# Kernel tuning notes

Measured on AMD Instinct MI355X. Metric: run time of the kernel, lower is better.

Reference implementation:

```python
import jax, jax.numpy as jnp
import numpy as np

N = 50000      # nodes
E = 800000     # edges (avg degree 16)
F_IN = 256     # input features
H = 128        # hidden
C = 40         # classes


def setup_inputs() -> dict:
    key = jax.random.key(0)
    ks = jax.random.split(key, 10)
    features = jax.random.normal(ks[0], (N, F_IN), dtype=jnp.float32)
    src = jax.random.randint(ks[1], (E,), 0, N, dtype=jnp.int32)
    dst = jax.random.randint(ks[2], (E,), 0, N, dtype=jnp.int32)
    edge_weights = jax.random.uniform(ks[3], (E,), dtype=jnp.float32)
    def glorot(k, i, o):
        return jax.random.normal(k, (i, o), dtype=jnp.float32) * np.float32(1.0 / np.sqrt(i))
    W1 = glorot(ks[4], F_IN, H); b1 = jnp.zeros((H,), jnp.float32)
    W2 = glorot(ks[5], H, H);    b2 = jnp.zeros((H,), jnp.float32)
    W3 = glorot(ks[6], H, C);    b3 = jnp.zeros((C,), jnp.float32)
    return dict(features=features, src=src, dst=dst, edge_weights=edge_weights,
                W1=W1, b1=b1, W2=W2, b2=b2, W3=W3, b3=b3)


def _gcn_layer(h, src, dst, ew, out_norm, in_norm, W, b, act):
    # norm='both': pre-scale by out_degree^-0.5, post-scale by in_degree^-0.5
    h = h * out_norm[:, None]
    in_gt_out = W.shape[0] > W.shape[1]
    if in_gt_out:
        h = h @ W                      # matmul first (in_feats > out_feats)
    # message = u_mul_e, reduce = sum  (SpMM-style gather-scale-scatter)
    agg = jax.ops.segment_sum(h[src] * ew[:, None], dst, num_segments=N)
    if not in_gt_out:
        agg = agg @ W                  # aggregate first (in_feats <= out_feats)
    agg = agg * in_norm[:, None] + b
    return act(agg) if act is not None else agg


def reference(features, src, dst, edge_weights, W1, b1, W2, b2, W3, b3):
    ones = jnp.ones((E,), jnp.float32)
    out_deg = jnp.clip(jax.ops.segment_sum(ones, src, num_segments=N), 1.0)
    in_deg = jnp.clip(jax.ops.segment_sum(ones, dst, num_segments=N), 1.0)
    out_norm = out_deg ** -0.5
    in_norm = in_deg ** -0.5
    relu = jax.nn.relu
    # dropout is identity in eval mode
    h = _gcn_layer(features, src, dst, edge_weights, out_norm, in_norm, W1, b1, relu)
    h = _gcn_layer(h, src, dst, edge_weights, out_norm, in_norm, W2, b2, relu)
    h = _gcn_layer(h, src, dst, edge_weights, out_norm, in_norm, W3, b3, None)
    return h
```

## Files before the change

kernel.cpp:

```cpp
#include <hip/hip_runtime.h>
#include <hip/hip_bf16.h>
#include <cstdint>


#define F_IN 256
#define HDIM 128
#define CDIM 40
#define RBITS 13
#define RSIZE 8192
#define NSUB 64

typedef short bf16x8 __attribute__((ext_vector_type(8)));
typedef float f32x4  __attribute__((ext_vector_type(4)));

__device__ __forceinline__ ushort f2bf(float x) {
    uint b = __float_as_uint(x);
    return (ushort)((b + 0x7fffu + ((b >> 16) & 1u)) >> 16);
}
__device__ __forceinline__ float bf2f(ushort h) {
    return __uint_as_float(((uint)h) << 16);
}

__global__ __launch_bounds__(256)
void histo_range(const int* __restrict__ src, const int* __restrict__ dst,
                 int* __restrict__ pc, int E) {
    __shared__ int h[RSIZE];
    const int s = blockIdx.x;
    const int r = blockIdx.y;
    const int base = r << RBITS;
    const int t = threadIdx.x;
    int4* h4 = reinterpret_cast<int4*>(h);
    for (int j = t; j < RSIZE / 4; j += 256) h4[j] = make_int4(0, 0, 0, 0);
    __syncthreads();

    const int ech = (E + NSUB - 1) / NSUB;
    const int e0 = s * ech;
    const int e1 = min(E, e0 + ech);
    const int n4 = (e1 - e0) >> 2;
    for (int g = t; g < n4; g += 256) {
        int4 d4 = *reinterpret_cast<const int4*>(dst + e0 + g * 4);
        int4 s4 = *reinterpret_cast<const int4*>(src + e0 + g * 4);
        #pragma unroll
        for (int j = 0; j < 4; ++j) {
            int d = (&d4.x)[j] - base;
            int v = (&s4.x)[j] - base;
            if ((unsigned)d < RSIZE) atomicAdd(&h[d], 1);
            if ((unsigned)v < RSIZE) atomicAdd(&h[v], 0x10000);
        }
    }
    for (int e = e0 + n4 * 4 + t; e < e1; e += 256) {
        int d = dst[e] - base, v = src[e] - base;
        if ((unsigned)d < RSIZE) atomicAdd(&h[d], 1);
        if ((unsigned)v < RSIZE) atomicAdd(&h[v], 0x10000);
    }
    __syncthreads();
    int* p = pc + ((size_t)r * NSUB + s) * RSIZE;
    for (int j = t; j < RSIZE; j += 256) p[j] = h[j];
}

__global__ __launch_bounds__(256)
void scan_blocks(const int* __restrict__ pc, int* __restrict__ out,
                 int* __restrict__ bsums, int n) {
    const int t = threadIdx.x;
    const int idx = blockIdx.x * 1024 + t * 4;
    int4 v = make_int4(0, 0, 0, 0);
    if (idx + 3 < n) {
        const int r = idx >> RBITS, off = idx & (RSIZE - 1);
        const int* p = pc + (size_t)r * NSUB * RSIZE + off;
        #pragma unroll 8
        for (int c = 0; c < NSUB; ++c) {
            int4 u = *reinterpret_cast<const int4*>(p + (size_t)c * RSIZE);
            v.x += u.x & 0xffff; v.y += u.y & 0xffff;
            v.z += u.z & 0xffff; v.w += u.w & 0xffff;
        }
    } else {
        for (int j = 0; j < 4; ++j) {
            if (idx + j < n) {
                const int r = (idx + j) >> RBITS, off = (idx + j) & (RSIZE - 1);
                int s = 0;
                for (int c = 0; c < NSUB; ++c)
                    s += pc[(size_t)r * NSUB * RSIZE + (size_t)c * RSIZE + off] & 0xffff;
                (&v.x)[j] = s;
            }
        }
    }
    const int s = v.x + v.y + v.z + v.w;
    const int lane = t & 63;
    int incl = s;
    #pragma unroll
    for (int off = 1; off < 64; off <<= 1) {
        int u = __shfl_up(incl, off);
        if (lane >= off) incl += u;
    }
    __shared__ int wsum[4];
    if (lane == 63) wsum[t >> 6] = incl;
    __syncthreads();
    const int w = t >> 6;
    int woff = 0;
    if (w > 0) woff += wsum[0];
    if (w > 1) woff += wsum[1];
    if (w > 2) woff += wsum[2];
    const int excl = woff + incl - s;
    if (idx + 3 < n) {
        *reinterpret_cast<int4*>(out + idx) =
            make_int4(excl, excl + v.x, excl + v.x + v.y, excl + v.x + v.y + v.z);
    } else {
        if (idx     < n) out[idx]     = excl;
        if (idx + 1 < n) out[idx + 1] = excl + v.x;
        if (idx + 2 < n) out[idx + 2] = excl + v.x + v.y;
        if (idx + 3 < n) out[idx + 3] = excl + v.x + v.y + v.z;
    }
    if (t == 255) bsums[blockIdx.x] = woff + incl;
}

__global__ __launch_bounds__(64)
void scan_sums(int* __restrict__ bsums, int nb) {
    const int lane = threadIdx.x & 63;
    int carry = 0;
    for (int base = 0; base < nb; base += 64) {
        int v = (base + lane < nb) ? bsums[base + lane] : 0;
        int incl = v;
        #pragma unroll
        for (int off = 1; off < 64; off <<= 1) {
            int u = __shfl_up(incl, off);
            if (lane >= off) incl += u;
        }
        if (base + lane < nb) bsums[base + lane] = carry + incl - v;
        carry += __shfl(incl, 63);
    }
}

__global__ __launch_bounds__(256)
void node_prep_kernel(const int* __restrict__ pc,
                      int* __restrict__ row_ptr, const int* __restrict__ bsums,
                      float* __restrict__ out_norm, float* __restrict__ in_norm,
                      int* __restrict__ cb, int n, int E) {
    int i = blockIdx.x * 256 + threadIdx.x;
    if (i < n) {
        const int r = i >> RBITS, off = i & (RSIZE - 1);
        const int* p = pc + (size_t)r * NSUB * RSIZE + off;
        int rp = row_ptr[i] + bsums[i >> 10];
        row_ptr[i] = rp;
        int cur = rp;
        int od = 0;
        #pragma unroll 8
        for (int c = 0; c < NSUB; ++c) {
            unsigned pv = (unsigned)p[(size_t)c * RSIZE];
            cb[(size_t)c * n + i] = cur;
            cur += (int)(pv & 0xffffu);
            od  += (int)(pv >> 16);
        }
        int id = cur - rp;
        out_norm[i] = rsqrtf((float)max(od, 1));
        in_norm[i]  = rsqrtf((float)max(id, 1));
    }
    if (i == 0) row_ptr[n] = E;
}

__global__ __launch_bounds__(256)
void scatter_range(const int* __restrict__ src, const int* __restrict__ dst,
                   const float* __restrict__ ew, const float* __restrict__ out_norm,
                   const int* __restrict__ cb, int2* __restrict__ edges,
                   int E, int N) {
    __shared__ int cur[RSIZE];
    const int s = blockIdx.x;
    const int r = blockIdx.y;
    const int base = r << RBITS;
    const int t = threadIdx.x;
    for (int j = t; j < RSIZE; j += 256)
        if (base + j < N) cur[j] = cb[(size_t)s * N + base + j];
    __syncthreads();

    const int ech = (E + NSUB - 1) / NSUB;
    const int e0 = s * ech;
    const int e1 = min(E, e0 + ech);
    const int n4 = (e1 - e0) >> 2;
    for (int g = t; g < n4; g += 256) {
        int4 d4 = *reinterpret_cast<const int4*>(dst + e0 + g * 4);
        int4 s4 = *reinterpret_cast<const int4*>(src + e0 + g * 4);
        float4 w4 = *reinterpret_cast<const float4*>(ew + e0 + g * 4);
        #pragma unroll
        for (int j = 0; j < 4; ++j) {
            int d = (&d4.x)[j] - base;
            if ((unsigned)d < RSIZE) {
                int sv = (&s4.x)[j];
                int pos = atomicAdd(&cur[d], 1);
                float w = (&w4.x)[j] * out_norm[sv];
                edges[pos] = make_int2(sv, __float_as_int(w));
            }
        }
    }
    for (int e = e0 + n4 * 4 + t; e < e1; e += 256) {
        int d = dst[e] - base;
        if ((unsigned)d < RSIZE) {
            int sv = src[e];
            int pos = atomicAdd(&cur[d], 1);
            float w = ew[e] * out_norm[sv];
            edges[pos] = make_int2(sv, __float_as_int(w));
        }
    }
}

__global__ __launch_bounds__(256)
void conv_w(const float* __restrict__ W, ushort* __restrict__ Wt_hi,
            ushort* __restrict__ Wt_lo, int K) {
    int i = blockIdx.x * 256 + threadIdx.x;
    if (i < K * 128) {
        int k = i >> 7, n = i & 127;
        float x = W[i];
        ushort hi = f2bf(x);
        ushort lo = f2bf(x - bf2f(hi));
        Wt_hi[(size_t)n * K + k] = hi;
        Wt_lo[(size_t)n * K + k] = lo;
    }
}

template <int MODE>
__global__ __launch_bounds__(256)
void gemm128_mfma(const float* __restrict__ A, const ushort* __restrict__ Wt_hi,
                  const ushort* __restrict__ Wt_lo, float* __restrict__ C,
                  int M, int K,
                  const float* __restrict__ rownorm, const float* __restrict__ bias) {
    constexpr int BK = 32;
    constexpr int AP = 40;
    __shared__ __align__(16) ushort As_hi[64 * AP];
    __shared__ __align__(16) ushort As_lo[64 * AP];
    __shared__ __align__(16) ushort Bs_hi[128 * AP];
    __shared__ __align__(16) ushort Bs_lo[128 * AP];

    const int t = threadIdx.x;
    const int w = t >> 6;
    const int l = t & 63;
    const int row0 = blockIdx.x * 64;

    const int ar = t >> 2;
    const int ak = (t & 3) * 8;
    const int bn = t >> 1;
    const int bko = (t & 1) * 16;

    const int fr = l & 15;
    const int fk = (l >> 4) * 8;

    f32x4 acc[8];
    #pragma unroll
    for (int i = 0; i < 8; ++i) acc[i] = (f32x4){0.f, 0.f, 0.f, 0.f};

    const bool arow_ok = (row0 + ar < M);
    const float* ap = A + (size_t)(row0 + ar) * K;

    for (int k0 = 0; k0 < K; k0 += BK) {
        float av[8];
        if (arow_ok) {
            float4 f0 = *reinterpret_cast<const float4*>(ap + k0 + ak);
            float4 f1 = *reinterpret_cast<const float4*>(ap + k0 + ak + 4);
            av[0] = f0.x; av[1] = f0.y; av[2] = f0.z; av[3] = f0.w;
            av[4] = f1.x; av[5] = f1.y; av[6] = f1.z; av[7] = f1.w;
        } else {
            #pragma unroll
            for (int j = 0; j < 8; ++j) av[j] = 0.f;
        }
        bf16x8 ah, al;
        #pragma unroll
        for (int j = 0; j < 8; ++j) {
            ushort hi = f2bf(av[j]);
            ah[j] = (short)hi;
            al[j] = (short)f2bf(av[j] - bf2f(hi));
        }
        const ushort* wh = Wt_hi + (size_t)bn * K + k0 + bko;
        const ushort* wl = Wt_lo + (size_t)bn * K + k0 + bko;
        bf16x8 bh0 = *reinterpret_cast<const bf16x8*>(wh);
        bf16x8 bh1 = *reinterpret_cast<const bf16x8*>(wh + 8);
        bf16x8 bl0 = *reinterpret_cast<const bf16x8*>(wl);
        bf16x8 bl1 = *reinterpret_cast<const bf16x8*>(wl + 8);

        __syncthreads();
        *reinterpret_cast<bf16x8*>(As_hi + ar * AP + ak) = ah;
        *reinterpret_cast<bf16x8*>(As_lo + ar * AP + ak) = al;
        *reinterpret_cast<bf16x8*>(Bs_hi + bn * AP + bko)     = bh0;
        *reinterpret_cast<bf16x8*>(Bs_hi + bn * AP + bko + 8) = bh1;
        *reinterpret_cast<bf16x8*>(Bs_lo + bn * AP + bko)     = bl0;
        *reinterpret_cast<bf16x8*>(Bs_lo + bn * AP + bko + 8) = bl1;
        __syncthreads();

        bf16x8 a_hi = *reinterpret_cast<const bf16x8*>(As_hi + (w * 16 + fr) * AP + fk);
        bf16x8 a_lo = *reinterpret_cast<const bf16x8*>(As_lo + (w * 16 + fr) * AP + fk);
        #pragma unroll
        for (int nt = 0; nt < 8; ++nt) {
            bf16x8 b_hi = *reinterpret_cast<const bf16x8*>(Bs_hi + (nt * 16 + fr) * AP + fk);
            bf16x8 b_lo = *reinterpret_cast<const bf16x8*>(Bs_lo + (nt * 16 + fr) * AP + fk);
            acc[nt] = __builtin_amdgcn_mfma_f32_16x16x32_bf16(a_hi, b_hi, acc[nt], 0, 0, 0);
            acc[nt] = __builtin_amdgcn_mfma_f32_16x16x32_bf16(a_hi, b_lo, acc[nt], 0, 0, 0);
            acc[nt] = __builtin_amdgcn_mfma_f32_16x16x32_bf16(a_lo, b_hi, acc[nt], 0, 0, 0);
        }
    }

    float bb[8];
    if (MODE == 1) {
        #pragma unroll
        for (int nt = 0; nt < 8; ++nt) bb[nt] = bias[nt * 16 + fr];
    }
    #pragma unroll
    for (int r = 0; r < 4; ++r) {
        int row = row0 + w * 16 + (l >> 4) * 4 + r;
        if (row >= M) continue;
        float rn = (MODE == 1) ? rownorm[row] : 0.f;
        float* cp = C + (size_t)row * 128;
        #pragma unroll
        for (int nt = 0; nt < 8; ++nt) {
            float v = acc[nt][r];
            if (MODE == 1) v = fmaxf(fmaf(v, rn, bb[nt]), 0.f);
            cp[nt * 16 + fr] = v;
        }
    }
}

template <int MODE>
__global__ __launch_bounds__(256)
void gemm_f32(const float* __restrict__ A, const float* __restrict__ B,
              float* __restrict__ C, int M, int Nn, int K,
              int lda, int ldb, int ldc,
              const float* __restrict__ rownorm, const float* __restrict__ bias) {
    constexpr int BM = 64, BN = 64, BK = 16;
    __shared__ float As[BK][BM + 4];
    __shared__ float Bs[BK][BN];

    const int t = threadIdx.x;
    const int row0 = blockIdx.x * BM;
    const int col0 = blockIdx.y * BN;
    const int rowbase = (t >> 4) * 4;
    const int colbase = (t & 15) * 4;
    const int ar  = t >> 2;
    const int akq = (t & 3) * 4;
    const int bk  = t >> 4;
    const int bc4 = (t & 15) * 4;

    float acc[4][4];
    #pragma unroll
    for (int i = 0; i < 4; ++i)
        #pragma unroll
        for (int j = 0; j < 4; ++j) acc[i][j] = 0.f;

    const bool arow_ok = (row0 + ar < M);
    const bool bcol_ok = (col0 + bc4 < Nn);
    const float* ap = A + (size_t)(row0 + ar) * lda + akq;

    float4 a0 = make_float4(0.f, 0.f, 0.f, 0.f), bv = a0;
    if (arow_ok) a0 = *reinterpret_cast<const float4*>(ap);
    if (bcol_ok)
        bv = *reinterpret_cast<const float4*>(B + (size_t)bk * ldb + col0 + bc4);

    for (int k0 = 0; k0 < K; k0 += BK) {
        __syncthreads();
        As[akq + 0][ar] = a0.x;
        As[akq + 1][ar] = a0.y;
        As[akq + 2][ar] = a0.z;
        As[akq + 3][ar] = a0.w;
        *reinterpret_cast<float4*>(&Bs[bk][bc4]) = bv;
        __syncthreads();

        if (k0 + BK < K) {
            if (arow_ok) a0 = *reinterpret_cast<const float4*>(ap + k0 + BK);
            if (bcol_ok)
                bv = *reinterpret_cast<const float4*>(B + (size_t)(k0 + BK + bk) * ldb + col0 + bc4);
        }

        #pragma unroll
        for (int kk = 0; kk < BK; ++kk) {
            float4 av  = *reinterpret_cast<const float4*>(&As[kk][rowbase]);
            float4 bv2 = *reinterpret_cast<const float4*>(&Bs[kk][colbase]);
            float a[4] = {av.x, av.y, av.z, av.w};
            float b[4] = {bv2.x, bv2.y, bv2.z, bv2.w};
            #pragma unroll
            for (int i = 0; i < 4; ++i)
                #pragma unroll
                for (int j = 0; j < 4; ++j)
                    acc[i][j] = fmaf(a[i], b[j], acc[i][j]);
        }
    }

    if (col0 + colbase >= Nn) return;
    float4 bb = make_float4(0.f, 0.f, 0.f, 0.f);
    if (MODE == 1) bb = *reinterpret_cast<const float4*>(bias + col0 + colbase);
    #pragma unroll
    for (int i = 0; i < 4; ++i) {
        int row = row0 + rowbase + i;
        if (row >= M) break;
        float4 v = make_float4(acc[i][0], acc[i][1], acc[i][2], acc[i][3]);
        if (MODE == 1) {
            float rn = rownorm[row];
            v.x = fmaxf(fmaf(v.x, rn, bb.x), 0.f);
            v.y = fmaxf(fmaf(v.y, rn, bb.y), 0.f);
            v.z = fmaxf(fmaf(v.z, rn, bb.z), 0.f);
            v.w = fmaxf(fmaf(v.w, rn, bb.w), 0.f);
        }
        *reinterpret_cast<float4*>(C + (size_t)row * ldc + col0 + colbase) = v;
    }
}

template <int EPI>
__global__ __launch_bounds__(256)
void spmm128(const float* __restrict__ H, const int* __restrict__ row_ptr,
             const int2* __restrict__ edges,
             float* __restrict__ out, const float* __restrict__ in_norm,
             const float* __restrict__ bias, int n) {
    constexpr int CAP = 1024;
    __shared__ int2 sh_e[CAP];
    const int t = threadIdx.x;
    const int w = t >> 6;
    const int lane = t & 63;
    const int quarter = lane >> 4;
    const int q = lane & 15;
    const int wid = blockIdx.x * 4 + w;
    const int nb4 = min(blockIdx.x * 4 + 4, n);
    const int e_begin = row_ptr[blockIdx.x * 4];
    const int e_end   = row_ptr[nb4];
    int ew0 = 0, ew1 = 0;
    if (wid < n) { ew0 = row_ptr[wid]; ew1 = row_ptr[wid + 1]; }

    float4 acc0 = make_float4(0.f, 0.f, 0.f, 0.f);
    float4 acc1 = make_float4(0.f, 0.f, 0.f, 0.f);

    for (int done = e_begin; done < e_end; done += CAP) {
        const int cnt = min(CAP, e_end - done);
        __syncthreads();
        for (int j = t; j < cnt; j += 256) sh_e[j] = edges[done + j];
        __syncthreads();
        const int lo = max(ew0, done), hi = min(ew1, done + cnt);
        int e = lo + ((quarter - (lo - ew0)) & 3);
        #pragma unroll 4
        for (; e < hi; e += 4) {
            int2 er = sh_e[e - done];
            int   s = er.x;
            float wv = __int_as_float(er.y);
            const float* hp = H + (size_t)s * 128 + q * 4;
            float4 v0 = *reinterpret_cast<const float4*>(hp);
            float4 v1 = *reinterpret_cast<const float4*>(hp + 64);
            acc0.x = fmaf(wv, v0.x, acc0.x); acc0.y = fmaf(wv, v0.y, acc0.y);
            acc0.z = fmaf(wv, v0.z, acc0.z); acc0.w = fmaf(wv, v0.w, acc0.w);
            acc1.x = fmaf(wv, v1.x, acc1.x); acc1.y = fmaf(wv, v1.y, acc1.y);
            acc1.z = fmaf(wv, v1.z, acc1.z); acc1.w = fmaf(wv, v1.w, acc1.w);
        }
    }

    #pragma unroll
    for (int d = 16; d <= 32; d <<= 1) {
        acc0.x += __shfl_xor(acc0.x, d); acc0.y += __shfl_xor(acc0.y, d);
        acc0.z += __shfl_xor(acc0.z, d); acc0.w += __shfl_xor(acc0.w, d);
        acc1.x += __shfl_xor(acc1.x, d); acc1.y += __shfl_xor(acc1.y, d);
        acc1.z += __shfl_xor(acc1.z, d); acc1.w += __shfl_xor(acc1.w, d);
    }
    if (wid < n && quarter == 0) {
        if (EPI == 1) {
            float nn = in_norm[wid];
            float4 bb0 = *reinterpret_cast<const float4*>(bias + q * 4);
            float4 bb1 = *reinterpret_cast<const float4*>(bias + 64 + q * 4);
            acc0.x = fmaxf(fmaf(acc0.x, nn, bb0.x), 0.f);
            acc0.y = fmaxf(fmaf(acc0.y, nn, bb0.y), 0.f);
            acc0.z = fmaxf(fmaf(acc0.z, nn, bb0.z), 0.f);
            acc0.w = fmaxf(fmaf(acc0.w, nn, bb0.w), 0.f);
            acc1.x = fmaxf(fmaf(acc1.x, nn, bb1.x), 0.f);
            acc1.y = fmaxf(fmaf(acc1.y, nn, bb1.y), 0.f);
            acc1.z = fmaxf(fmaf(acc1.z, nn, bb1.z), 0.f);
            acc1.w = fmaxf(fmaf(acc1.w, nn, bb1.w), 0.f);
        }
        float* op = out + (size_t)wid * 128 + q * 4;
        *reinterpret_cast<float4*>(op)      = acc0;
        *reinterpret_cast<float4*>(op + 64) = acc1;
    }
}

__global__ __launch_bounds__(256)
void spmm40(const float* __restrict__ H, const int* __restrict__ row_ptr,
            const int2* __restrict__ edges,
            float* __restrict__ out, const float* __restrict__ in_norm,
            const float* __restrict__ bias, int n) {
    constexpr int CAP = 1024;
    __shared__ int2 sh_e[CAP];
    const int t = threadIdx.x;
    const int w = t >> 6;
    const int lane = t & 63;
    const int quarter = lane >> 4;
    const int q = lane & 15;
    const int wid = blockIdx.x * 4 + w;
    const int nb4 = min(blockIdx.x * 4 + 4, n);
    const int e_begin = row_ptr[blockIdx.x * 4];
    const int e_end   = row_ptr[nb4];
    int ew0 = 0, ew1 = 0;
    if (wid < n) { ew0 = row_ptr[wid]; ew1 = row_ptr[wid + 1]; }

    float4 acc = make_float4(0.f, 0.f, 0.f, 0.f);

    for (int done = e_begin; done < e_end; done += CAP) {
        const int cnt = min(CAP, e_end - done);
        __syncthreads();
        for (int j = t; j < cnt; j += 256) sh_e[j] = edges[done + j];
        __syncthreads();
        const int lo = max(ew0, done), hi = min(ew1, done + cnt);
        int e = lo + ((quarter - (lo - ew0)) & 3);
        #pragma unroll 4
        for (; e < hi; e += 4) {
            int2 er = sh_e[e - done];
            int   s = er.x;
            float wv = __int_as_float(er.y);
            float4 v = *reinterpret_cast<const float4*>(H + (size_t)s * 64 + q * 4);
            acc.x = fmaf(wv, v.x, acc.x);
            acc.y = fmaf(wv, v.y, acc.y);
            acc.z = fmaf(wv, v.z, acc.z);
            acc.w = fmaf(wv, v.w, acc.w);
        }
    }

    #pragma unroll
    for (int d = 16; d <= 32; d <<= 1) {
        acc.x += __shfl_xor(acc.x, d);
        acc.y += __shfl_xor(acc.y, d);
        acc.z += __shfl_xor(acc.z, d);
        acc.w += __shfl_xor(acc.w, d);
    }
    if (wid < n && quarter == 0 && q * 4 < CDIM) {
        float nn = in_norm[wid];
        float4 bb = *reinterpret_cast<const float4*>(bias + q * 4);
        acc.x = fmaf(acc.x, nn, bb.x);
        acc.y = fmaf(acc.y, nn, bb.y);
        acc.z = fmaf(acc.z, nn, bb.z);
        acc.w = fmaf(acc.w, nn, bb.w);
        *reinterpret_cast<float4*>(out + (size_t)wid * CDIM + q * 4) = acc;
    }
}


extern "C" void kernel_launch(void* const* d_in, const int* in_sizes, int n_in,
                              void* d_out, int out_size, void* d_ws, size_t ws_size,
                              hipStream_t stream) {
    const float* features = (const float*)d_in[0];
    const int*   src      = (const int*)d_in[1];
    const int*   dst      = (const int*)d_in[2];
    const float* ew       = (const float*)d_in[3];
    const float* W1       = (const float*)d_in[4];
    const float* b1       = (const float*)d_in[5];
    const float* W2       = (const float*)d_in[6];
    const float* b2       = (const float*)d_in[7];
    const float* W3       = (const float*)d_in[8];
    const float* b3       = (const float*)d_in[9];
    float* out = (float*)d_out;

    const int N = in_sizes[0] / F_IN;
    const int E = in_sizes[1];
    const int NR = (N + RSIZE - 1) >> RBITS;

    char* ws = (char*)d_ws;
    size_t off = 0;
    auto alloc = [&](size_t bytes) -> void* {
        void* p = ws + off;
        off += (bytes + 255) & ~(size_t)255;
        return p;
    };
    int*    row_ptr  = (int*)alloc((size_t)(N + 1) * 4);
    float*  out_norm = (float*)alloc((size_t)N * 4);
    float*  in_norm  = (float*)alloc((size_t)N * 4);
    int2*   edges    = (int2*)alloc((size_t)E * 8);
    float*  B0       = (float*)alloc((size_t)N * HDIM * 4);
    float*  B1       = (float*)alloc((size_t)N * HDIM * 4);
    float*  B2       = (float*)alloc((size_t)N * HDIM * 4);
    const int nb     = (N + 1023) / 1024;
    int*    bsums    = (int*)alloc((size_t)nb * 4);
    ushort* Wt1_hi   = (ushort*)alloc((size_t)F_IN * 128 * 2);
    ushort* Wt1_lo   = (ushort*)alloc((size_t)F_IN * 128 * 2);
    ushort* Wt2_hi   = (ushort*)alloc((size_t)HDIM * 128 * 2);
    ushort* Wt2_lo   = (ushort*)alloc((size_t)HDIM * 128 * 2);
    int*    pc       = (int*)B0;
    int*    cb       = (int*)B1;
    (void)ws_size;

    {
        dim3 grid(NSUB, NR);
        histo_range<<<grid, 256, 0, stream>>>(src, dst, pc, E);
    }
    conv_w<<<(F_IN * 128 + 255) / 256, 256, 0, stream>>>(W1, Wt1_hi, Wt1_lo, F_IN);
    conv_w<<<(HDIM * 128 + 255) / 256, 256, 0, stream>>>(W2, Wt2_hi, Wt2_lo, HDIM);
    scan_blocks<<<nb, 256, 0, stream>>>(pc, row_ptr, bsums, N);
    scan_sums<<<1, 64, 0, stream>>>(bsums, nb);
    int ngrid = (N + 255) / 256;
    node_prep_kernel<<<ngrid, 256, 0, stream>>>(pc, row_ptr, bsums,
                                                out_norm, in_norm, cb, N, E);
    {
        dim3 grid(NSUB, NR);
        scatter_range<<<grid, 256, 0, stream>>>(src, dst, ew, out_norm, cb,
                                                edges, E, N);
    }

    const int spmm_grid = (N + 3) / 4;
    const int ggrid = (N + 63) / 64;

    gemm128_mfma<0><<<ggrid, 256, 0, stream>>>(features, Wt1_hi, Wt1_lo, B0,
                                               N, F_IN, nullptr, nullptr);
    spmm128<1><<<spmm_grid, 256, 0, stream>>>(B0, row_ptr, edges, B1, in_norm, b1, N);

    spmm128<0><<<spmm_grid, 256, 0, stream>>>(B1, row_ptr, edges, B2, nullptr, nullptr, N);
    gemm128_mfma<1><<<ggrid, 256, 0, stream>>>(B2, Wt2_hi, Wt2_lo, B0,
                                               N, HDIM, in_norm, b2);

    {
        dim3 grid(ggrid, 1);
        gemm_f32<0><<<grid, 256, 0, stream>>>(B0, W3, B1, N, CDIM, HDIM,
                                              HDIM, CDIM, 64, nullptr, nullptr);
    }
    spmm40<<<spmm_grid, 256, 0, stream>>>(B1, row_ptr, edges, out, in_norm, b3, N);
}
```

Measured before the change: 250.3 us.

## Split SpMM wavefronts into eight edge groups with software-pipelined row prefetch

Both SpMM kernels now let each wavefront process eight edges at a time instead of four, with eight lanes per edge each loading 16 (or 8) contiguous floats. The next edge's row is also loaded before the current one is accumulated, so more gathers are in flight. The aim is to hide gather latency for the irregular neighbour reads, which bound this memory-latency-dominated step. In exchange it uses more registers, adds a third shuffle-reduction stage, and loads less coalesced contiguous segments per lane. In spmm40 it also reads beyond column 40 in the 64-wide padded rows, as before.

```diff
diff --git a/kernel.cpp b/kernel.cpp
--- a/kernel.cpp
+++ b/kernel.cpp
@@ -408,8 +408,8 @@
     const int t = threadIdx.x;
     const int w = t >> 6;
     const int lane = t & 63;
-    const int quarter = lane >> 4;
-    const int q = lane & 15;
+    const int oct = lane >> 3;
+    const int o   = lane & 7;
     const int wid = blockIdx.x * 4 + w;
     const int nb4 = min(blockIdx.x * 4 + 4, n);
     const int e_begin = row_ptr[blockIdx.x * 4];
@@ -418,7 +418,7 @@
     if (wid < n) { ew0 = row_ptr[wid]; ew1 = row_ptr[wid + 1]; }
 
     float4 acc0 = make_float4(0.f, 0.f, 0.f, 0.f);
-    float4 acc1 = make_float4(0.f, 0.f, 0.f, 0.f);
+    float4 acc1 = acc0, acc2 = acc0, acc3 = acc0;
 
     for (int done = e_begin; done < e_end; done += CAP) {
         const int cnt = min(CAP, e_end - done);
@@ -426,34 +426,62 @@
         for (int j = t; j < cnt; j += 256) sh_e[j] = edges[done + j];
         __syncthreads();
         const int lo = max(ew0, done), hi = min(ew1, done + cnt);
-        int e = lo + ((quarter - (lo - ew0)) & 3);
-        #pragma unroll 4
-        for (; e < hi; e += 4) {
-            int2 er = sh_e[e - done];
-            int   s = er.x;
-            float wv = __int_as_float(er.y);
-            const float* hp = H + (size_t)s * 128 + q * 4;
-            float4 v0 = *reinterpret_cast<const float4*>(hp);
-            float4 v1 = *reinterpret_cast<const float4*>(hp + 64);
-            acc0.x = fmaf(wv, v0.x, acc0.x); acc0.y = fmaf(wv, v0.y, acc0.y);
-            acc0.z = fmaf(wv, v0.z, acc0.z); acc0.w = fmaf(wv, v0.w, acc0.w);
-            acc1.x = fmaf(wv, v1.x, acc1.x); acc1.y = fmaf(wv, v1.y, acc1.y);
-            acc1.z = fmaf(wv, v1.z, acc1.z); acc1.w = fmaf(wv, v1.w, acc1.w);
+        int e = lo + ((oct - (lo - ew0)) & 7);
+        int2 er = make_int2(0, 0);
+        float4 c0, c1, c2, c3;
+        if (e < hi) {
+            er = sh_e[e - done];
+            const float* hp = H + (size_t)er.x * 128 + o * 16;
+            c0 = *reinterpret_cast<const float4*>(hp);
+            c1 = *reinterpret_cast<const float4*>(hp + 4);
+            c2 = *reinterpret_cast<const float4*>(hp + 8);
+            c3 = *reinterpret_cast<const float4*>(hp + 12);
+        }
+        while (e < hi) {
+            const int en = e + 8;
+            int2 ern = make_int2(0, 0);
+            float4 p0, p1, p2, p3;
+            if (en < hi) {
+                ern = sh_e[en - done];
+                const float* hp2 = H + (size_t)ern.x * 128 + o * 16;
+                p0 = *reinterpret_cast<const float4*>(hp2);
+                p1 = *reinterpret_cast<const float4*>(hp2 + 4);
+                p2 = *reinterpret_cast<const float4*>(hp2 + 8);
+                p3 = *reinterpret_cast<const float4*>(hp2 + 12);
+            }
+            const float wv = __int_as_float(er.y);
+            acc0.x = fmaf(wv, c0.x, acc0.x); acc0.y = fmaf(wv, c0.y, acc0.y);
+            acc0.z = fmaf(wv, c0.z, acc0.z); acc0.w = fmaf(wv, c0.w, acc0.w);
+            acc1.x = fmaf(wv, c1.x, acc1.x); acc1.y = fmaf(wv, c1.y, acc1.y);
+            acc1.z = fmaf(wv, c1.z, acc1.z); acc1.w = fmaf(wv, c1.w, acc1.w);
+            acc2.x = fmaf(wv, c2.x, acc2.x); acc2.y = fmaf(wv, c2.y, acc2.y);
+            acc2.z = fmaf(wv, c2.z, acc2.z); acc2.w = fmaf(wv, c2.w, acc2.w);
+            acc3.x = fmaf(wv, c3.x, acc3.x); acc3.y = fmaf(wv, c3.y, acc3.y);
+            acc3.z = fmaf(wv, c3.z, acc3.z); acc3.w = fmaf(wv, c3.w, acc3.w);
+            e = en; er = ern;
+            c0 = p0; c1 = p1; c2 = p2; c3 = p3;
         }
     }
 
     #pragma unroll
-    for (int d = 16; d <= 32; d <<= 1) {
+    for (int d = 8; d <= 32; d <<= 1) {
         acc0.x += __shfl_xor(acc0.x, d); acc0.y += __shfl_xor(acc0.y, d);
         acc0.z += __shfl_xor(acc0.z, d); acc0.w += __shfl_xor(acc0.w, d);
         acc1.x += __shfl_xor(acc1.x, d); acc1.y += __shfl_xor(acc1.y, d);
         acc1.z += __shfl_xor(acc1.z, d); acc1.w += __shfl_xor(acc1.w, d);
-    }
-    if (wid < n && quarter == 0) {
+        acc2.x += __shfl_xor(acc2.x, d); acc2.y += __shfl_xor(acc2.y, d);
+        acc2.z += __shfl_xor(acc2.z, d); acc2.w += __shfl_xor(acc2.w, d);
+        acc3.x += __shfl_xor(acc3.x, d); acc3.y += __shfl_xor(acc3.y, d);
+        acc3.z += __shfl_xor(acc3.z, d); acc3.w += __shfl_xor(acc3.w, d);
+    }
+    if (wid < n && oct == 0) {
         if (EPI == 1) {
             float nn = in_norm[wid];
-            float4 bb0 = *reinterpret_cast<const float4*>(bias + q * 4);
-            float4 bb1 = *reinterpret_cast<const float4*>(bias + 64 + q * 4);
+            const float* bp = bias + o * 16;
+            float4 bb0 = *reinterpret_cast<const float4*>(bp);
+            float4 bb1 = *reinterpret_cast<const float4*>(bp + 4);
+            float4 bb2 = *reinterpret_cast<const float4*>(bp + 8);
+            float4 bb3 = *reinterpret_cast<const float4*>(bp + 12);
             acc0.x = fmaxf(fmaf(acc0.x, nn, bb0.x), 0.f);
             acc0.y = fmaxf(fmaf(acc0.y, nn, bb0.y), 0.f);
             acc0.z = fmaxf(fmaf(acc0.z, nn, bb0.z), 0.f);
@@ -462,10 +490,20 @@
             acc1.y = fmaxf(fmaf(acc1.y, nn, bb1.y), 0.f);
             acc1.z = fmaxf(fmaf(acc1.z, nn, bb1.z), 0.f);
             acc1.w = fmaxf(fmaf(acc1.w, nn, bb1.w), 0.f);
-        }
-        float* op = out + (size_t)wid * 128 + q * 4;
+            acc2.x = fmaxf(fmaf(acc2.x, nn, bb2.x), 0.f);
+            acc2.y = fmaxf(fmaf(acc2.y, nn, bb2.y), 0.f);
+            acc2.z = fmaxf(fmaf(acc2.z, nn, bb2.z), 0.f);
+            acc2.w = fmaxf(fmaf(acc2.w, nn, bb2.w), 0.f);
+            acc3.x = fmaxf(fmaf(acc3.x, nn, bb3.x), 0.f);
+            acc3.y = fmaxf(fmaf(acc3.y, nn, bb3.y), 0.f);
+            acc3.z = fmaxf(fmaf(acc3.z, nn, bb3.z), 0.f);
+            acc3.w = fmaxf(fmaf(acc3.w, nn, bb3.w), 0.f);
+        }
+        float* op = out + (size_t)wid * 128 + o * 16;
         *reinterpret_cast<float4*>(op)      = acc0;
-        *reinterpret_cast<float4*>(op + 64) = acc1;
+        *reinterpret_cast<float4*>(op + 4)  = acc1;
+        *reinterpret_cast<float4*>(op + 8)  = acc2;
+        *reinterpret_cast<float4*>(op + 12) = acc3;
     }
 }
 
@@ -479,8 +517,8 @@
     const int t = threadIdx.x;
     const int w = t >> 6;
     const int lane = t & 63;
-    const int quarter = lane >> 4;
-    const int q = lane & 15;
+    const int oct = lane >> 3;
+    const int o   = lane & 7;
     const int wid = blockIdx.x * 4 + w;
     const int nb4 = min(blockIdx.x * 4 + 4, n);
     const int e_begin = row_ptr[blockIdx.x * 4];
@@ -488,7 +526,8 @@
     int ew0 = 0, ew1 = 0;
     if (wid < n) { ew0 = row_ptr[wid]; ew1 = row_ptr[wid + 1]; }
 
-    float4 acc = make_float4(0.f, 0.f, 0.f, 0.f);
+    float4 acc0 = make_float4(0.f, 0.f, 0.f, 0.f);
+    float4 acc1 = acc0;
 
     for (int done = e_begin; done < e_end; done += CAP) {
         const int cnt = min(CAP, e_end - done);
@@ -496,35 +535,58 @@
         for (int j = t; j < cnt; j += 256) sh_e[j] = edges[done + j];
         __syncthreads();
         const int lo = max(ew0, done), hi = min(ew1, done + cnt);
-        int e = lo + ((quarter - (lo - ew0)) & 3);
-        #pragma unroll 4
-        for (; e < hi; e += 4) {
-            int2 er = sh_e[e - done];
-            int   s = er.x;
-            float wv = __int_as_float(er.y);
-            float4 v = *reinterpret_cast<const float4*>(H + (size_t)s * 64 + q * 4);
-            acc.x = fmaf(wv, v.x, acc.x);
-            acc.y = fmaf(wv, v.y, acc.y);
-            acc.z = fmaf(wv, v.z, acc.z);
-            acc.w = fmaf(wv, v.w, acc.w);
+        int e = lo + ((oct - (lo - ew0)) & 7);
+        int2 er = make_int2(0, 0);
+        float4 c0, c1;
+        if (e < hi) {
+            er = sh_e[e - done];
+            const float* hp = H + (size_t)er.x * 64 + o * 8;
+            c0 = *reinterpret_cast<const float4*>(hp);
+            c1 = *reinterpret_cast<const float4*>(hp + 4);
+        }
+        while (e < hi) {
+            const int en = e + 8;
+            int2 ern = make_int2(0, 0);
+            float4 p0, p1;
+            if (en < hi) {
+                ern = sh_e[en - done];
+                const float* hp2 = H + (size_t)ern.x * 64 + o * 8;
+                p0 = *reinterpret_cast<const float4*>(hp2);
+                p1 = *reinterpret_cast<const float4*>(hp2 + 4);
+            }
+            const float wv = __int_as_float(er.y);
+            acc0.x = fmaf(wv, c0.x, acc0.x); acc0.y = fmaf(wv, c0.y, acc0.y);
+            acc0.z = fmaf(wv, c0.z, acc0.z); acc0.w = fmaf(wv, c0.w, acc0.w);
+            acc1.x = fmaf(wv, c1.x, acc1.x); acc1.y = fmaf(wv, c1.y, acc1.y);
+            acc1.z = fmaf(wv, c1.z, acc1.z); acc1.w = fmaf(wv, c1.w, acc1.w);
+            e = en; er = ern;
+            c0 = p0; c1 = p1;
         }
     }
 
     #pragma unroll
-    for (int d = 16; d <= 32; d <<= 1) {
-        acc.x += __shfl_xor(acc.x, d);
-        acc.y += __shfl_xor(acc.y, d);
-        acc.z += __shfl_xor(acc.z, d);
-        acc.w += __shfl_xor(acc.w, d);
-    }
-    if (wid < n && quarter == 0 && q * 4 < CDIM) {
+    for (int d = 8; d <= 32; d <<= 1) {
+        acc0.x += __shfl_xor(acc0.x, d); acc0.y += __shfl_xor(acc0.y, d);
+        acc0.z += __shfl_xor(acc0.z, d); acc0.w += __shfl_xor(acc0.w, d);
+        acc1.x += __shfl_xor(acc1.x, d); acc1.y += __shfl_xor(acc1.y, d);
+        acc1.z += __shfl_xor(acc1.z, d); acc1.w += __shfl_xor(acc1.w, d);
+    }
+    if (wid < n && oct == 0 && o * 8 < CDIM) {
         float nn = in_norm[wid];
-        float4 bb = *reinterpret_cast<const float4*>(bias + q * 4);
-        acc.x = fmaf(acc.x, nn, bb.x);
-        acc.y = fmaf(acc.y, nn, bb.y);
-        acc.z = fmaf(acc.z, nn, bb.z);
-        acc.w = fmaf(acc.w, nn, bb.w);
-        *reinterpret_cast<float4*>(out + (size_t)wid * CDIM + q * 4) = acc;
+        const float* bp = bias + o * 8;
+        float4 bb0 = *reinterpret_cast<const float4*>(bp);
+        float4 bb1 = *reinterpret_cast<const float4*>(bp + 4);
+        acc0.x = fmaf(acc0.x, nn, bb0.x);
+        acc0.y = fmaf(acc0.y, nn, bb0.y);
+        acc0.z = fmaf(acc0.z, nn, bb0.z);
+        acc0.w = fmaf(acc0.w, nn, bb0.w);
+        acc1.x = fmaf(acc1.x, nn, bb1.x);
+        acc1.y = fmaf(acc1.y, nn, bb1.y);
+        acc1.z = fmaf(acc1.z, nn, bb1.z);
+        acc1.w = fmaf(acc1.w, nn, bb1.w);
+        float* op = out + (size_t)wid * CDIM + o * 8;
+        *reinterpret_cast<float4*>(op)     = acc0;
+        *reinterpret_cast<float4*>(op + 4) = acc1;
     }
 }
 
```

New measurement: 250.5 us. Within noise of the previous version (+0.1%).
